# Optimization experiments

Hardware: AMD Instinct MI355X
Metric: run time of the kernel (lower is better)

## Reference

```python
import jax, jax.numpy as jnp
import numpy as np

AABB0 = np.array([-1.5, -1.5, -1.5], np.float32)
AABB1 = np.array([1.5, 1.5, 1.5], np.float32)
GRID = (300, 300, 300)
NEAR, FAR = 2.0, 6.0
STEP = float(np.mean((AABB1 - AABB0) / (np.array(GRID, np.float32) - 1)) * 0.5)  # step_ratio=0.5
DIST_SCALE = 25.0
DENSITY_SHIFT = -10.0
W_THRES = 1e-4
PE = 2  # view_pe = feat_pe = 2
MAT = ((0, 1), (0, 2), (1, 2))
VEC = (2, 1, 0)
N_RAYS, N_SAMP = 1024, 512
DN, AN = 16, 16
APP_DIM, FEAT_C = 27, 128
IN_MLP = 2 * PE * 3 + 2 * PE * APP_DIM + 3 + APP_DIM  # 150


def posenc(x, freqs):
    fb = (2.0 ** jnp.arange(freqs)).astype(x.dtype)
    p = (x[..., None] * fb).reshape(x.shape[:-1] + (x.shape[-1] * freqs,))
    return jnp.concatenate([jnp.sin(p), jnp.cos(p)], -1)


def bilinear2d(plane, xy):
    # plane [C,H,W]; xy [P,2] in [-1,1], x->W, y->H; align_corners=True, border clamp
    C, H, W = plane.shape
    x = jnp.clip((xy[:, 0] * 0.5 + 0.5) * (W - 1), 0.0, W - 1)
    y = jnp.clip((xy[:, 1] * 0.5 + 0.5) * (H - 1), 0.0, H - 1)
    x0 = jnp.clip(jnp.floor(x), 0, W - 2).astype(jnp.int32)
    y0 = jnp.clip(jnp.floor(y), 0, H - 2).astype(jnp.int32)
    wx, wy = x - x0, y - y0
    v00 = plane[:, y0, x0]
    v01 = plane[:, y0, x0 + 1]
    v10 = plane[:, y0 + 1, x0]
    v11 = plane[:, y0 + 1, x0 + 1]
    return (v00 * (1 - wx) + v01 * wx) * (1 - wy) + (v10 * (1 - wx) + v11 * wx) * wy  # [C,P]


def linear1d(line, z):
    # line [C,L]; z [P] in [-1,1]
    C, L = line.shape
    t = jnp.clip((z * 0.5 + 0.5) * (L - 1), 0.0, L - 1)
    i0 = jnp.clip(jnp.floor(t), 0, L - 2).astype(jnp.int32)
    w = t - i0
    return line[:, i0] * (1 - w) + line[:, i0 + 1] * w  # [C,P]


def _forward(rays_o, rays_d, dplanes, dlines, aplanes, alines, basis_w,
             w1, b1, w2, b2, w3, b3, n_samples):
    a0, a1 = jnp.asarray(AABB0), jnp.asarray(AABB1)
    # --- sample_ray (is_train=False) ---
    vec = jnp.where(rays_d == 0, 1e-6, rays_d)
    rate_a = (a1 - rays_o) / vec
    rate_b = (a0 - rays_o) / vec
    t_min = jnp.clip(jnp.max(jnp.minimum(rate_a, rate_b), -1), NEAR, FAR)  # [R]
    rng = jnp.arange(n_samples, dtype=rays_o.dtype)[None]
    z_vals = t_min[:, None] + STEP * rng  # [R,S]
    pts = rays_o[:, None, :] + rays_d[:, None, :] * z_vals[..., None]  # [R,S,3]
    ray_valid = jnp.all((pts >= a0) & (pts <= a1), -1)  # [R,S]
    xn = ((pts - a0) * (2.0 / (a1 - a0)) - 1.0).reshape(-1, 3)  # normalize_coord -> [P,3]
    # --- density: VM decomposition (sum of plane*line products) ---
    sigma_feat = jnp.zeros((xn.shape[0],), xn.dtype)
    for i in range(3):
        p = bilinear2d(dplanes[i], xn[:, jnp.array(MAT[i])])
        l = linear1d(dlines[i], xn[:, VEC[i]])
        sigma_feat = sigma_feat + jnp.sum(p * l, 0)
    sigma = jax.nn.softplus(sigma_feat + DENSITY_SHIFT).reshape(z_vals.shape)
    sigma = jnp.where(ray_valid, sigma, 0.0)
    # --- raw2alpha compositing ---
    dists = jnp.concatenate([z_vals[:, 1:] - z_vals[:, :-1], jnp.zeros_like(z_vals[:, :1])], -1)
    alpha = 1.0 - jnp.exp(-sigma * dists * DIST_SCALE)
    T = jnp.cumprod(jnp.concatenate([jnp.ones_like(alpha[:, :1]), 1.0 - alpha + 1e-10], -1), -1)
    weight = alpha * T[:, :-1]
    app_mask = weight > W_THRES
    # --- appearance features + basis_mat ---
    coefs = [bilinear2d(aplanes[i], xn[:, jnp.array(MAT[i])]) * linear1d(alines[i], xn[:, VEC[i]])
             for i in range(3)]
    feat = jnp.concatenate(coefs, 0).T @ basis_w.T  # [P, app_dim]
    view = jnp.broadcast_to(rays_d[:, None, :], pts.shape).reshape(-1, 3)
    # --- MLPRender_Fea: [features, viewdirs, posenc(features), posenc(viewdirs)] ---
    mlp_in = jnp.concatenate([feat, view, posenc(feat, PE), posenc(view, PE)], -1)
    h = jax.nn.relu(mlp_in @ w1.T + b1)
    h = jax.nn.relu(h @ w2.T + b2)
    rgb = jax.nn.sigmoid(h @ w3.T + b3).reshape(z_vals.shape + (3,))
    rgb = jnp.where(app_mask[..., None], rgb, 0.0)
    acc = jnp.sum(weight, -1)
    rgb_map = jnp.sum(weight[..., None] * rgb, 1)
    rgb_map = jnp.clip(rgb_map + (1.0 - acc)[:, None], 0.0, 1.0)  # white background
    depth_map = jnp.sum(weight * z_vals, -1)
    return rgb_map, depth_map


def setup_inputs() -> dict:
    key = jax.random.key(0)
    ks = jax.random.split(key, 20)
    rd = jax.random.normal(ks[0], (N_RAYS, 3), jnp.float32)
    rays_d = rd / jnp.linalg.norm(rd, axis=-1, keepdims=True)
    rays_o = -3.0 * rays_d + 0.1 * jax.random.normal(ks[1], (N_RAYS, 3), jnp.float32)
    inp = {"rays_o": rays_o, "rays_d": rays_d}
    for i, ((m0, m1), v) in enumerate(zip(MAT, VEC)):
        inp[f"dplane{i}"] = jax.random.normal(ks[2 + i], (DN, GRID[m1], GRID[m0]), jnp.float32)
        inp[f"dline{i}"] = jax.random.normal(ks[5 + i], (DN, GRID[v]), jnp.float32)
        inp[f"aplane{i}"] = 0.1 * jax.random.normal(ks[8 + i], (AN, GRID[m1], GRID[m0]), jnp.float32)
        inp[f"aline{i}"] = 0.1 * jax.random.normal(ks[11 + i], (AN, GRID[v]), jnp.float32)
    inp["basis_w"] = 0.1 * jax.random.normal(ks[14], (APP_DIM, 3 * AN), jnp.float32)
    inp["w1"] = 0.05 * jax.random.normal(ks[15], (FEAT_C, IN_MLP), jnp.float32)
    inp["b1"] = jnp.zeros((FEAT_C,), jnp.float32)
    inp["w2"] = 0.05 * jax.random.normal(ks[16], (FEAT_C, FEAT_C), jnp.float32)
    inp["b2"] = jnp.zeros((FEAT_C,), jnp.float32)
    inp["w3"] = 0.05 * jax.random.normal(ks[17], (3, FEAT_C), jnp.float32)
    inp["b3"] = jnp.zeros((3,), jnp.float32)
    inp["n_samples"] = N_SAMP
    return inp


def reference(rays_o, rays_d, dplane0, dplane1, dplane2, dline0, dline1, dline2,
              aplane0, aplane1, aplane2, aline0, aline1, aline2, basis_w,
              w1, b1, w2, b2, w3, b3, n_samples):
    return _forward(rays_o, rays_d, (dplane0, dplane1, dplane2), (dline0, dline1, dline2),
                    (aplane0, aplane1, aplane2), (aline0, aline1, aline2), basis_w,
                    w1, b1, w2, b2, w3, b3, n_samples)
```

## Files before the change

kernel.cpp:

```cpp
#include <hip/hip_runtime.h>
#include <hip/hip_fp16.h>
#include <math.h>

#define NRAYS 1024
#define NSAMP 512
#define GRIDN 300
#define POS_ELEMS (GRIDN*GRIDN)
#define PLANE_ELEMS (16*POS_ELEMS)
#define CMAX 524288

typedef short bf16x8 __attribute__((ext_vector_type(8)));
typedef short short8 __attribute__((ext_vector_type(8)));
typedef float f32x4  __attribute__((ext_vector_type(4)));

struct H8v { __half2 h[4]; };

__device__ __forceinline__ float clampf(float x, float a, float b){ return fminf(fmaxf(x,a),b); }
__device__ __forceinline__ unsigned short f2b(float f){
    unsigned u = __builtin_bit_cast(unsigned, f);
    u = (u + 0x7FFFu + ((u>>16)&1u)) >> 16;
    return (unsigned short)u;
}
__device__ __forceinline__ float b2f(unsigned short h){
    unsigned u = ((unsigned)h) << 16;
    return __builtin_bit_cast(float, u);
}

__device__ __forceinline__ float ray_tmin(float o0,float o1,float o2,float d0,float d1,float d2){
    float v0=(d0==0.f)?1e-6f:d0, v1=(d1==0.f)?1e-6f:d1, v2=(d2==0.f)?1e-6f:d2;
    float t_min = -1e30f, a, b;
    a=(1.5f-o0)/v0; b=(-1.5f-o0)/v0; t_min=fmaxf(t_min,fminf(a,b));
    a=(1.5f-o1)/v1; b=(-1.5f-o1)/v1; t_min=fmaxf(t_min,fminf(a,b));
    a=(1.5f-o2)/v2; b=(-1.5f-o2)/v2; t_min=fmaxf(t_min,fminf(a,b));
    return clampf(t_min, 2.0f, 6.0f);
}

struct TPtrs {
    const float* psrc[6]; __half* pdst[6];
    const float* lsrc[6]; __half* ldst[6];
};

__global__ __launch_bounds__(256) void k_transpose(TPtrs tp) {
    int by  = blockIdx.y;
    int pos = blockIdx.x * 256 + threadIdx.x;
    if (pos < POS_ELEMS) {
        const float* src = tp.psrc[by];
        __half2 o[8];
        #pragma unroll
        for (int e = 0; e < 8; e++) {
            float a = src[(2*e  ) * POS_ELEMS + pos];
            float b = src[(2*e+1) * POS_ELEMS + pos];
            o[e] = __float22half2_rn(make_float2(a,b));
        }
        float4* dst = (float4*)(tp.pdst[by] + (size_t)pos * 16);
        dst[0] = *(float4*)&o[0];
        dst[1] = *(float4*)&o[4];
    }
    if (pos < GRIDN) {
        const float* ls = tp.lsrc[by];
        __half*      ld = tp.ldst[by];
        #pragma unroll
        for (int c = 0; c < 16; c++) ld[pos * 16 + c] = __float2half_rn(ls[c * GRIDN + pos]);
    }
}

__global__ __launch_bounds__(256) void k_prepw(
    const float* __restrict__ w1, const float* __restrict__ w2,
    unsigned short* __restrict__ w1b, unsigned short* __restrict__ w2b)
{
    int idx = blockIdx.x * 256 + threadIdx.x;
    if (idx < 128*160) {
        int j = idx / 160, k = idx - j*160;
        w1b[idx] = (k < 150) ? f2b(w1[j*150 + k]) : 0;
    } else if (idx < 128*160 + 128*128) {
        int i2 = idx - 128*160;
        w2b[i2] = f2b(w2[i2]);
    }
}

__global__ __launch_bounds__(256) void k_alpha(
    const float* __restrict__ ro, const float* __restrict__ rd,
    const __half* __restrict__ dpT0, const __half* __restrict__ dpT1, const __half* __restrict__ dpT2,
    const __half* __restrict__ dlT0, const __half* __restrict__ dlT1, const __half* __restrict__ dlT2,
    float* __restrict__ alpha_out)
{
    const float STEPF = (3.0f/299.0f)*0.5f;
    int gid = blockIdx.x*256 + threadIdx.x;
    int id = gid >> 1, h = gid & 1;
    int r = id >> 9, s = id & (NSAMP-1);

    float o0=ro[r*3+0], o1=ro[r*3+1], o2=ro[r*3+2];
    float d0=rd[r*3+0], d1=rd[r*3+1], d2=rd[r*3+2];
    float t_min = ray_tmin(o0,o1,o2,d0,d1,d2);

    float z  = t_min + STEPF * (float)s;
    float p0 = o0 + d0*z, p1 = o1 + d1*z, p2 = o2 + d2*z;
    bool valid = (p0>=-1.5f)&&(p0<=1.5f)&&(p1>=-1.5f)&&(p1<=1.5f)&&(p2>=-1.5f)&&(p2<=1.5f);

    float sfp = 0.f;
    if (valid) {
        float xn[3] = { (p0+1.5f)*(2.0f/3.0f)-1.0f,
                        (p1+1.5f)*(2.0f/3.0f)-1.0f,
                        (p2+1.5f)*(2.0f/3.0f)-1.0f };
        const __half* dpT[3] = {dpT0,dpT1,dpT2};
        const __half* dlT[3] = {dlT0,dlT1,dlT2};
        const int M0[3]={0,0,1}, M1[3]={1,2,2}, V[3]={2,1,0};
        #pragma unroll
        for (int i=0;i<3;i++) {
            float fx = clampf((xn[M0[i]]*0.5f+0.5f)*299.f, 0.f, 299.f);
            float fy = clampf((xn[M1[i]]*0.5f+0.5f)*299.f, 0.f, 299.f);
            float ft = clampf((xn[V[i]] *0.5f+0.5f)*299.f, 0.f, 299.f);
            int x0=min((int)fx,298), y0=min((int)fy,298), i0=min((int)ft,298);
            float wx=fx-(float)x0, wy=fy-(float)y0, wt=ft-(float)i0;
            __half2 w00=__float2half2_rn((1.f-wx)*(1.f-wy)), w01=__float2half2_rn(wx*(1.f-wy));
            __half2 w10=__float2half2_rn((1.f-wx)*wy),       w11=__float2half2_rn(wx*wy);
            __half2 u0 =__float2half2_rn(1.f-wt),            u1 =__float2half2_rn(wt);
            const __half* base = dpT[i] + (size_t)(y0*GRIDN+x0)*16 + h*8;
            H8v a00 = *(const H8v*)(base);
            H8v a01 = *(const H8v*)(base + 16);
            H8v a10 = *(const H8v*)(base + GRIDN*16);
            H8v a11 = *(const H8v*)(base + GRIDN*16 + 16);
            const __half* lb = dlT[i] + (size_t)i0*16 + h*8;
            H8v l0 = *(const H8v*)(lb);
            H8v l1 = *(const H8v*)(lb + 16);
            #pragma unroll
            for (int e=0;e<4;e++) {
                __half2 p = __hmul2(a00.h[e],w00);
                p = __hfma2(a01.h[e],w01,p);
                p = __hfma2(a10.h[e],w10,p);
                p = __hfma2(a11.h[e],w11,p);
                __half2 l = __hmul2(l0.h[e],u0);
                l = __hfma2(l1.h[e],u1,l);
                float2 c = __half22float2(__hmul2(p,l));
                sfp += c.x + c.y;
            }
        }
    }
    float sf = sfp + __shfl_xor(sfp, 1, 64);
    if (h == 0) {
        float sig = 0.f;
        if (valid) {
            float xs = sf - 10.0f;
            sig = fmaxf(xs, 0.f) + __logf(1.f + __expf(-fabsf(xs)));
        }
        alpha_out[id] = (s < NSAMP-1) ? (1.f - __expf(-sig * (STEPF*25.0f))) : 0.f;
    }
}

__global__ __launch_bounds__(256) void k_scan(
    const float* __restrict__ ro, const float* __restrict__ rd,
    const float* __restrict__ alpha_in,
    float* __restrict__ acc_out, float* __restrict__ depth_out,
    int* __restrict__ tmpl, float* __restrict__ tmpw, int* __restrict__ cnt)
{
    const float STEPF = (3.0f/299.0f)*0.5f;
    int r = blockIdx.x;
    int tid = threadIdx.x;
    int lane = tid & 63, wv = tid >> 6;

    float o0=ro[r*3+0], o1=ro[r*3+1], o2=ro[r*3+2];
    float d0=rd[r*3+0], d1=rd[r*3+1], d2=rd[r*3+2];
    float t_min = ray_tmin(o0,o1,o2,d0,d1,d2);

    float2 av = *(const float2*)&alpha_in[r*NSAMP + 2*tid];
    float aj0 = av.x, aj1 = av.y;
    float zj0 = t_min + STEPF * (float)(2*tid);
    float zj1 = t_min + STEPF * (float)(2*tid+1);

    float v0 = (1.f - aj0) + 1e-10f;
    float v1 = (1.f - aj1) + 1e-10f;
    float inc = v0 * v1;
    #pragma unroll
    for (int off=1; off<64; off<<=1) {
        float t = __shfl_up(inc, off, 64);
        if (lane >= off) inc *= t;
    }
    __shared__ float wtot[4], swsum[4], sdep[4];
    __shared__ int   wcnt[4];
    if (lane == 63) wtot[wv] = inc;
    __syncthreads();
    float pre = 1.f;
    for (int i=0;i<wv;i++) pre *= wtot[i];
    float excl = __shfl_up(inc, 1, 64);
    if (lane == 0) excl = 1.f;
    float T0 = pre * excl;
    float w0 = aj0 * T0;
    float w1 = aj1 * T0 * v0;

    float rw = w0 + w1, rz = w0*zj0 + w1*zj1;
    #pragma unroll
    for (int off=32; off>0; off>>=1) { rw += __shfl_xor(rw,off,64); rz += __shfl_xor(rz,off,64); }
    if (lane == 0) { swsum[wv] = rw; sdep[wv] = rz; }

    bool act0 = (w0 > 1e-4f), act1 = (w1 > 1e-4f);
    unsigned long long m0 = __ballot(act0);
    unsigned long long m1 = __ballot(act1);
    int tot = __popcll(m0) + __popcll(m1);
    if (lane == 0) wcnt[wv] = tot;
    __syncthreads();
    int base = 0;
    for (int i=0;i<wv;i++) base += wcnt[i];
    unsigned long long below = (1ull<<lane)-1ull;
    int o = base + __popcll(m0 & below) + __popcll(m1 & below);
    int* tl = tmpl + r*NSAMP;
    float* tw = tmpw + r*NSAMP;
    if (act0) { tl[o] = (r<<9)|(2*tid);   tw[o] = w0; o++; }
    if (act1) { tl[o] = (r<<9)|(2*tid+1); tw[o] = w1; }

    if (tid == 0) {
        float a=0.f, b=0.f;
        #pragma unroll
        for (int i=0;i<4;i++){ a+=swsum[i]; b+=sdep[i]; }
        acc_out[r] = a; depth_out[r] = b;
        cnt[r] = wcnt[0]+wcnt[1]+wcnt[2]+wcnt[3];
    }
}

__global__ __launch_bounds__(1024) void k_prefix(
    const int* __restrict__ cnt, int* __restrict__ basep, int* __restrict__ counter)
{
    int tid = threadIdx.x;
    int lane = tid & 63, wv = tid >> 6;
    int v = cnt[tid];
    int inc = v;
    #pragma unroll
    for (int off=1; off<64; off<<=1) {
        int t = __shfl_up(inc, off, 64);
        if (lane >= off) inc += t;
    }
    __shared__ int wsum[16];
    if (lane == 63) wsum[wv] = inc;
    __syncthreads();
    int pre = 0;
    for (int i=0;i<wv;i++) pre += wsum[i];
    basep[tid] = pre + inc - v;
    if (tid == 1023) *counter = pre + inc;
}

__global__ __launch_bounds__(256) void k_compact(
    const int* __restrict__ tmpl, const float* __restrict__ tmpw,
    const int* __restrict__ cnt, const int* __restrict__ basep,
    int* __restrict__ list, float* __restrict__ wlist)
{
    int r = blockIdx.x;
    int n = cnt[r], b = basep[r];
    const int* tl = tmpl + r*NSAMP;
    const float* tw = tmpw + r*NSAMP;
    for (int j = threadIdx.x; j < n; j += 256) {
        list[b+j]  = tl[j];
        wlist[b+j] = tw[j];
    }
}

__global__ __launch_bounds__(256) void k_gather(
    const float* __restrict__ ro, const float* __restrict__ rd,
    const __half* __restrict__ apT0, const __half* __restrict__ apT1, const __half* __restrict__ apT2,
    const __half* __restrict__ alT0, const __half* __restrict__ alT1, const __half* __restrict__ alT2,
    const float* __restrict__ basis_w,
    const int* __restrict__ list, const int* __restrict__ counter,
    float* __restrict__ Xf)
{
    const float STEPF = (3.0f/299.0f)*0.5f;
    int gid = blockIdx.x*256 + threadIdx.x;
    int idx = gid >> 3, q = gid & 7;
    int count = *counter;
    if (idx >= count) return;

    int sid = list[idx];
    int r = sid >> 9, s = sid & (NSAMP-1);
    float o0=ro[r*3+0], o1=ro[r*3+1], o2=ro[r*3+2];
    float d0=rd[r*3+0], d1=rd[r*3+1], d2=rd[r*3+2];
    float t_min = ray_tmin(o0,o1,o2,d0,d1,d2);
    float z = t_min + STEPF*(float)s;
    float xn[3] = { ((o0+d0*z)+1.5f)*(2.0f/3.0f)-1.0f,
                    ((o1+d1*z)+1.5f)*(2.0f/3.0f)-1.0f,
                    ((o2+d2*z)+1.5f)*(2.0f/3.0f)-1.0f };

    bool active = (q < 6);
    int i = min(q >> 1, 2);
    int h = q & 1;

    float c8[8];
    {
        const __half* apT[3]={apT0,apT1,apT2};
        const __half* alT[3]={alT0,alT1,alT2};
        const int M0[3]={0,0,1}, M1[3]={1,2,2}, V[3]={2,1,0};
        float fx = clampf((xn[M0[i]]*0.5f+0.5f)*299.f, 0.f, 299.f);
        float fy = clampf((xn[M1[i]]*0.5f+0.5f)*299.f, 0.f, 299.f);
        float ft = clampf((xn[V[i]] *0.5f+0.5f)*299.f, 0.f, 299.f);
        int x0=min((int)fx,298), y0=min((int)fy,298), i0=min((int)ft,298);
        float wx=fx-(float)x0, wy=fy-(float)y0, wt=ft-(float)i0;
        __half2 w00=__float2half2_rn((1.f-wx)*(1.f-wy)), w01=__float2half2_rn(wx*(1.f-wy));
        __half2 w10=__float2half2_rn((1.f-wx)*wy),       w11=__float2half2_rn(wx*wy);
        __half2 u0 =__float2half2_rn(1.f-wt),            u1 =__float2half2_rn(wt);
        if (active) {
            const __half* base = apT[i] + (size_t)(y0*GRIDN+x0)*16 + h*8;
            H8v a00 = *(const H8v*)(base);
            H8v a01 = *(const H8v*)(base + 16);
            H8v a10 = *(const H8v*)(base + GRIDN*16);
            H8v a11 = *(const H8v*)(base + GRIDN*16 + 16);
            const __half* lb = alT[i] + (size_t)i0*16 + h*8;
            H8v l0 = *(const H8v*)(lb);
            H8v l1 = *(const H8v*)(lb + 16);
            #pragma unroll
            for (int e=0;e<4;e++) {
                __half2 p = __hmul2(a00.h[e],w00);
                p = __hfma2(a01.h[e],w01,p);
                p = __hfma2(a10.h[e],w10,p);
                p = __hfma2(a11.h[e],w11,p);
                __half2 l = __hmul2(l0.h[e],u0);
                l = __hfma2(l1.h[e],u1,l);
                float2 c = __half22float2(__hmul2(p,l));
                c8[2*e]   = c.x;
                c8[2*e+1] = c.y;
            }
        } else {
            #pragma unroll
            for (int e=0;e<8;e++) c8[e] = 0.f;
        }
    }

    float kv[4] = {0.f, 0.f, 0.f, 0.f};
    #pragma unroll
    for (int j=0;j<27;j++) {
        const float4* b4 = (const float4*)(basis_w + j*48 + i*16 + h*8);
        float4 b0 = b4[0], b1 = b4[1];
        float p = b0.x*c8[0] + b0.y*c8[1] + b0.z*c8[2] + b0.w*c8[3]
                + b1.x*c8[4] + b1.y*c8[5] + b1.z*c8[6] + b1.w*c8[7];
        p += __shfl_xor(p, 1, 64);
        p += __shfl_xor(p, 2, 64);
        p += __shfl_xor(p, 4, 64);
        if (q == (j >> 2)) kv[j & 3] = p;
    }

    float4 v = make_float4(kv[0], kv[1], kv[2], kv[3]);
    if (q == 6) v.w = d0;
    if (q == 7) { v = make_float4(d1, d2, 0.f, 0.f); }
    *(float4*)&Xf[(size_t)idx*32 + q*4] = v;
}

#define XST 168
#define HST 136
#define TIL 32
#define XFS 36

__global__ __launch_bounds__(512, 4) void k_gemm(
    const float* __restrict__ Xf,
    const unsigned short* __restrict__ w1b, const float* __restrict__ b1p,
    const unsigned short* __restrict__ w2b, const float* __restrict__ b2p,
    const float* __restrict__ w3p, const float* __restrict__ b3p,
    const float* __restrict__ wlist, const int* __restrict__ counter,
    __half* __restrict__ contrib)
{
    __shared__ __align__(16) unsigned short Xs[TIL*XST];
    __shared__ __align__(16) unsigned short Hs[TIL*HST];
    __shared__ __align__(16) float Xf_s[2][TIL][XFS];

    int tid  = threadIdx.x;
    int wvid = tid >> 6, lane = tid & 63, ln15 = lane & 15, kq = lane >> 4;

    int count  = *counter;
    int ntiles = (count + TIL-1) >> 5;
    if ((int)blockIdx.x >= ntiles) return;

    int jrow = (wvid<<4) + ln15;
    bf16x8 w1f[5], w2f[4];
    #pragma unroll
    for (int ks=0; ks<5; ks++)
        w1f[ks] = *(const bf16x8*)&w1b[jrow*160 + ks*32 + kq*8];
    #pragma unroll
    for (int ks=0; ks<4; ks++)
        w2f[ks] = *(const bf16x8*)&w2b[jrow*128 + ks*32 + kq*8];
    float bias1 = b1p[jrow];
    float bias2 = b2p[jrow];

    int srow = tid >> 3, sq = tid & 7;

    int cur = 0;
    {
        if (tid < TIL*8) {
            int idx = blockIdx.x*TIL + srow;
            float4 v = make_float4(0.f,0.f,0.f,0.f);
            if (idx < count) v = *(const float4*)&Xf[(size_t)idx*32 + sq*4];
            *(float4*)&Xf_s[0][srow][sq*4] = v;
        }
        __syncthreads();
    }

    for (int t = blockIdx.x; t < ntiles; t += gridDim.x) {
        int tn = t + gridDim.x;
        bool havepf = (tn < ntiles) && (tid < TIL*8);
        float4 pf = make_float4(0.f,0.f,0.f,0.f);
        if (havepf) {
            int idx = tn*TIL + srow;
            if (idx < count) pf = *(const float4*)&Xf[(size_t)idx*32 + sq*4];
        }

        for (int u = tid; u < TIL*30; u += 512) {
            int row = u / 30, j = u - row*30;
            unsigned short* X = &Xs[row*XST];
            float f = Xf_s[cur][row][j];
            float s1 = __sinf(f), s2 = __sinf(2.f*f);
            float c1 = __cosf(f), c2 = __cosf(2.f*f);
            int c = j - 27;
            int o_s = (j < 27) ? (30 + 2*j) : (138 + 2*c);
            int o_c = (j < 27) ? (84 + 2*j) : (144 + 2*c);
            X[o_s]   = f2b(s1); X[o_s+1] = f2b(s2);
            X[o_c]   = f2b(c1); X[o_c+1] = f2b(c2);
            if ((j & 1) == 0) {
                float fB = Xf_s[cur][row][j+1];
                unsigned pk = (unsigned)f2b(f) | ((unsigned)f2b(fB) << 16);
                *(unsigned*)&X[j] = pk;
            }
        }
        for (int u = tid; u < TIL*10; u += 512) {
            int row = u / 10, k = 150 + (u - row*10);
            Xs[row*XST + k] = 0;
        }
        __syncthreads();

        {
            f32x4 acc[2] = {};
            #pragma unroll
            for (int ks=0; ks<5; ks++) {
                int ko = ks*32 + kq*8;
                #pragma unroll
                for (int m=0;m<2;m++) {
                    bf16x8 a = *(const bf16x8*)&Xs[(m*16 + ln15)*XST + ko];
                    acc[m] = __builtin_amdgcn_mfma_f32_16x16x32_bf16(a, w1f[ks], acc[m], 0,0,0);
                }
            }
            int col = jrow;
            #pragma unroll
            for (int m=0;m<2;m++) {
                int rbase = m*16 + kq*4;
                #pragma unroll
                for (int j=0;j<4;j++)
                    Hs[(rbase+j)*HST + col] = f2b(fmaxf(acc[m][j] + bias1, 0.f));
            }
        }
        __syncthreads();

        {
            f32x4 acc[2] = {};
            #pragma unroll
            for (int ks=0; ks<4; ks++) {
                int ko = ks*32 + kq*8;
                #pragma unroll
                for (int m=0;m<2;m++) {
                    bf16x8 a = *(const bf16x8*)&Hs[(m*16 + ln15)*HST + ko];
                    acc[m] = __builtin_amdgcn_mfma_f32_16x16x32_bf16(a, w2f[ks], acc[m], 0,0,0);
                }
            }
            int col = jrow;
            #pragma unroll
            for (int m=0;m<2;m++) {
                int rbase = m*16 + kq*4;
                #pragma unroll
                for (int j=0;j<4;j++)
                    Xs[(rbase+j)*HST + col] = f2b(fmaxf(acc[m][j] + bias2, 0.f));
            }
        }
        __syncthreads();

        if (havepf)
            *(float4*)&Xf_s[cur^1][srow][sq*4] = pf;

        if (tid < TIL*8) {
            int u = tid >> 3, q = tid & 7;
            int idx = t*TIL + u;
            if (q < 6 && idx < count) {
                int ch = q >> 1, hf = q & 1;
                float wgt = wlist[idx];
                const unsigned short* h2 = Xs + u*HST + hf*64;
                const float* wr = w3p + ch*128 + hf*64;
                float pa[4] = {0.f, 0.f, 0.f, 0.f};
                #pragma unroll
                for (int kc=0;kc<8;kc++) {
                    bf16x8 hv = *(const bf16x8*)&h2[kc*8];
                    const float* wrk = wr + kc*8;
                    float tacc = 0.f;
                    #pragma unroll
                    for (int e=0;e<8;e++)
                        tacc += b2f((unsigned short)hv[e]) * wrk[e];
                    pa[kc & 3] += tacc;
                }
                float p = (pa[0] + pa[1]) + (pa[2] + pa[3]);
                p += __shfl_xor(p, 1, 64);
                if (hf == 0) {
                    float v = 0.f;
                    if (wgt > 0.f) {
                        float acc5 = b3p[ch] + p;
                        v = wgt * (1.f/(1.f + __expf(-acc5)));
                    }
                    contrib[(size_t)ch*CMAX + idx] = __float2half(v);
                }
            }
        }
        __syncthreads();
        cur ^= 1;
    }
}

__global__ __launch_bounds__(128) void k_rgbsum(
    const __half* __restrict__ contrib,
    const int* __restrict__ cnt, const int* __restrict__ basep,
    float* __restrict__ rgbacc)
{
    int r = blockIdx.x;
    int n = cnt[r], b = basep[r];
    int tid = threadIdx.x, lane = tid & 63, w = tid >> 6;
    float s0=0.f, s1=0.f, s2=0.f;
    for (int j = tid; j < n; j += 128) {
        s0 += __half2float(contrib[0*CMAX + b + j]);
        s1 += __half2float(contrib[1*CMAX + b + j]);
        s2 += __half2float(contrib[2*CMAX + b + j]);
    }
    #pragma unroll
    for (int off=32; off>0; off>>=1) {
        s0 += __shfl_xor(s0,off,64); s1 += __shfl_xor(s1,off,64); s2 += __shfl_xor(s2,off,64);
    }
    __shared__ float sh[3][2];
    if (lane == 0) { sh[0][w]=s0; sh[1][w]=s1; sh[2][w]=s2; }
    __syncthreads();
    if (tid == 0) {
        rgbacc[r*3+0] = sh[0][0]+sh[0][1];
        rgbacc[r*3+1] = sh[1][0]+sh[1][1];
        rgbacc[r*3+2] = sh[2][0]+sh[2][1];
    }
}

__global__ __launch_bounds__(256) void k_final(
    const float* __restrict__ rgbacc, const float* __restrict__ acc_out, float* __restrict__ out)
{
    int i = blockIdx.x*256 + threadIdx.x;
    if (i < NRAYS*3) {
        int r = i/3;
        out[i] = clampf(rgbacc[i] + (1.f - acc_out[r]), 0.f, 1.f);
    }
}

extern "C" void kernel_launch(void* const* d_in, const int* in_sizes, int n_in,
                              void* d_out, int out_size, void* d_ws, size_t ws_size,
                              hipStream_t stream)
{
    const float* ro = (const float*)d_in[0];
    const float* rd = (const float*)d_in[1];
    const float* dplane[3] = {(const float*)d_in[2],(const float*)d_in[6],(const float*)d_in[10]};
    const float* dline[3]  = {(const float*)d_in[3],(const float*)d_in[7],(const float*)d_in[11]};
    const float* aplane[3] = {(const float*)d_in[4],(const float*)d_in[8],(const float*)d_in[12]};
    const float* aline[3]  = {(const float*)d_in[5],(const float*)d_in[9],(const float*)d_in[13]};
    const float* basis_w = (const float*)d_in[14];
    const float* w1 = (const float*)d_in[15];
    const float* b1 = (const float*)d_in[16];
    const float* w2 = (const float*)d_in[17];
    const float* b2 = (const float*)d_in[18];
    const float* w3 = (const float*)d_in[19];
    const float* b3 = (const float*)d_in[20];
    float* out = (float*)d_out;

    char* ws = (char*)d_ws;
    int*    counter  = (int*)   (ws + 0);
    float*  rgbacc   = (float*) (ws + 256);
    float*  accb     = (float*) (ws + 12544);
    float*  wlist    = (float*) (ws + 16640);
    int*    list     = (int*)   (ws + 2113792);
    __half* planesT  = (__half*)(ws + 4210944);
    __half* linesT   = (__half*)(ws + 21490944);
    unsigned short* w1b = (unsigned short*)(ws + 21548544);
    unsigned short* w2b = (unsigned short*)(ws + 21589504);
    float*  alphab   = (float*) (ws + 21622272);
    int*    cntb     = (int*)   (ws + 23719424);
    int*    baseb    = (int*)   (ws + 23723520);
    int*    tmpl     = (int*)   (ws + 23727616);
    float*  tmpw     = (float*) (ws + 25824768);
    __half* contrib  = (__half*)(ws + 23727616);
    float*  Xf       = (float*) (ws + 27921920);


    TPtrs tp;
    for (int i=0;i<3;i++) {
        tp.psrc[i]   = dplane[i]; tp.pdst[i]   = planesT + (size_t)i*PLANE_ELEMS;
        tp.psrc[3+i] = aplane[i]; tp.pdst[3+i] = planesT + (size_t)(3+i)*PLANE_ELEMS;
        tp.lsrc[i]   = dline[i];  tp.ldst[i]   = linesT + i*(GRIDN*16);
        tp.lsrc[3+i] = aline[i];  tp.ldst[3+i] = linesT + (3+i)*(GRIDN*16);
    }
    dim3 tg((POS_ELEMS+255)/256, 6);
    hipLaunchKernelGGL(k_transpose, tg, dim3(256), 0, stream, tp);

    k_prepw<<<(128*160 + 128*128 + 255)/256, 256, 0, stream>>>(w1, w2, w1b, w2b);

    k_alpha<<<(NRAYS*NSAMP*2)/256, 256, 0, stream>>>(
        ro, rd,
        planesT + 0*(size_t)PLANE_ELEMS, planesT + 1*(size_t)PLANE_ELEMS, planesT + 2*(size_t)PLANE_ELEMS,
        linesT + 0*(GRIDN*16), linesT + 1*(GRIDN*16), linesT + 2*(GRIDN*16),
        alphab);

    k_scan<<<NRAYS, 256, 0, stream>>>(
        ro, rd, alphab, accb, out + NRAYS*3, tmpl, tmpw, cntb);

    k_prefix<<<1, 1024, 0, stream>>>(cntb, baseb, counter);

    k_compact<<<NRAYS, 256, 0, stream>>>(tmpl, tmpw, cntb, baseb, list, wlist);

    k_gather<<<(CMAX*8)/256, 256, 0, stream>>>(
        ro, rd,
        planesT + 3*(size_t)PLANE_ELEMS, planesT + 4*(size_t)PLANE_ELEMS, planesT + 5*(size_t)PLANE_ELEMS,
        linesT + 3*(GRIDN*16), linesT + 4*(GRIDN*16), linesT + 5*(GRIDN*16),
        basis_w, list, counter, Xf);

    k_gemm<<<1024, 512, 0, stream>>>(
        Xf, w1b, b1, w2b, b2, w3, b3,
        wlist, counter, contrib);

    k_rgbsum<<<NRAYS, 128, 0, stream>>>(contrib, cntb, baseb, rgbacc);

    k_final<<<(NRAYS*3+255)/256, 256, 0, stream>>>(rgbacc, accb, out);
}
```

Measured before the change: 101.2 us.

## Replace prefix-scan and compaction kernels with atomic base allocation in scan

```diff
diff --git a/kernel.cpp b/kernel.cpp
--- a/kernel.cpp
+++ b/kernel.cpp
@@ -66,9 +66,11 @@
 
 __global__ __launch_bounds__(256) void k_prepw(
     const float* __restrict__ w1, const float* __restrict__ w2,
-    unsigned short* __restrict__ w1b, unsigned short* __restrict__ w2b)
+    unsigned short* __restrict__ w1b, unsigned short* __restrict__ w2b,
+    int* __restrict__ counter)
 {
     int idx = blockIdx.x * 256 + threadIdx.x;
+    if (idx == 0) *counter = 0;
     if (idx < 128*160) {
         int j = idx / 160, k = idx - j*160;
         w1b[idx] = (k < 150) ? f2b(w1[j*150 + k]) : 0;
@@ -151,7 +153,8 @@
     const float* __restrict__ ro, const float* __restrict__ rd,
     const float* __restrict__ alpha_in,
     float* __restrict__ acc_out, float* __restrict__ depth_out,
-    int* __restrict__ tmpl, float* __restrict__ tmpw, int* __restrict__ cnt)
+    int* __restrict__ list, float* __restrict__ wlist,
+    int* __restrict__ cnt, int* __restrict__ basep, int* __restrict__ counter)
 {
     const float STEPF = (3.0f/299.0f)*0.5f;
     int r = blockIdx.x;
@@ -177,6 +180,7 @@
     }
     __shared__ float wtot[4], swsum[4], sdep[4];
     __shared__ int   wcnt[4];
+    __shared__ int   sbase;
     if (lane == 63) wtot[wv] = inc;
     __syncthreads();
     float pre = 1.f;
@@ -198,57 +202,25 @@
     int tot = __popcll(m0) + __popcll(m1);
     if (lane == 0) wcnt[wv] = tot;
     __syncthreads();
-    int base = 0;
+
+    int btot = wcnt[0]+wcnt[1]+wcnt[2]+wcnt[3];
+    if (tid == 0) sbase = atomicAdd(counter, btot);
+    __syncthreads();
+
+    int base = sbase;
     for (int i=0;i<wv;i++) base += wcnt[i];
     unsigned long long below = (1ull<<lane)-1ull;
     int o = base + __popcll(m0 & below) + __popcll(m1 & below);
-    int* tl = tmpl + r*NSAMP;
-    float* tw = tmpw + r*NSAMP;
-    if (act0) { tl[o] = (r<<9)|(2*tid);   tw[o] = w0; o++; }
-    if (act1) { tl[o] = (r<<9)|(2*tid+1); tw[o] = w1; }
+    if (act0) { list[o] = (r<<9)|(2*tid);   wlist[o] = w0; o++; }
+    if (act1) { list[o] = (r<<9)|(2*tid+1); wlist[o] = w1; }
 
     if (tid == 0) {
         float a=0.f, b=0.f;
         #pragma unroll
         for (int i=0;i<4;i++){ a+=swsum[i]; b+=sdep[i]; }
         acc_out[r] = a; depth_out[r] = b;
-        cnt[r] = wcnt[0]+wcnt[1]+wcnt[2]+wcnt[3];
-    }
-}
-
-__global__ __launch_bounds__(1024) void k_prefix(
-    const int* __restrict__ cnt, int* __restrict__ basep, int* __restrict__ counter)
-{
-    int tid = threadIdx.x;
-    int lane = tid & 63, wv = tid >> 6;
-    int v = cnt[tid];
-    int inc = v;
-    #pragma unroll
-    for (int off=1; off<64; off<<=1) {
-        int t = __shfl_up(inc, off, 64);
-        if (lane >= off) inc += t;
-    }
-    __shared__ int wsum[16];
-    if (lane == 63) wsum[wv] = inc;
-    __syncthreads();
-    int pre = 0;
-    for (int i=0;i<wv;i++) pre += wsum[i];
-    basep[tid] = pre + inc - v;
-    if (tid == 1023) *counter = pre + inc;
-}
-
-__global__ __launch_bounds__(256) void k_compact(
-    const int* __restrict__ tmpl, const float* __restrict__ tmpw,
-    const int* __restrict__ cnt, const int* __restrict__ basep,
-    int* __restrict__ list, float* __restrict__ wlist)
-{
-    int r = blockIdx.x;
-    int n = cnt[r], b = basep[r];
-    const int* tl = tmpl + r*NSAMP;
-    const float* tw = tmpw + r*NSAMP;
-    for (int j = threadIdx.x; j < n; j += 256) {
-        list[b+j]  = tl[j];
-        wlist[b+j] = tw[j];
+        cnt[r] = btot;
+        basep[r] = sbase;
     }
 }
 
@@ -572,11 +544,8 @@
     float*  alphab   = (float*) (ws + 21622272);
     int*    cntb     = (int*)   (ws + 23719424);
     int*    baseb    = (int*)   (ws + 23723520);
-    int*    tmpl     = (int*)   (ws + 23727616);
-    float*  tmpw     = (float*) (ws + 25824768);
     __half* contrib  = (__half*)(ws + 23727616);
     float*  Xf       = (float*) (ws + 27921920);
-
 
     TPtrs tp;
     for (int i=0;i<3;i++) {
@@ -588,7 +557,7 @@
     dim3 tg((POS_ELEMS+255)/256, 6);
     hipLaunchKernelGGL(k_transpose, tg, dim3(256), 0, stream, tp);
 
-    k_prepw<<<(128*160 + 128*128 + 255)/256, 256, 0, stream>>>(w1, w2, w1b, w2b);
+    k_prepw<<<(128*160 + 128*128 + 255)/256, 256, 0, stream>>>(w1, w2, w1b, w2b, counter);
 
     k_alpha<<<(NRAYS*NSAMP*2)/256, 256, 0, stream>>>(
         ro, rd,
@@ -597,11 +566,7 @@
         alphab);
 
     k_scan<<<NRAYS, 256, 0, stream>>>(
-        ro, rd, alphab, accb, out + NRAYS*3, tmpl, tmpw, cntb);
-
-    k_prefix<<<1, 1024, 0, stream>>>(cntb, baseb, counter);
-
-    k_compact<<<NRAYS, 256, 0, stream>>>(tmpl, tmpw, cntb, baseb, list, wlist);
+        ro, rd, alphab, accb, out + NRAYS*3, list, wlist, cntb, baseb, counter);
 
     k_gather<<<(CMAX*8)/256, 256, 0, stream>>>(
         ro, rd,
```

Measured after the change: 106.3 us. +5.0%, slower.
